# Kernel optimization log

Hardware: AMD Instinct MI355X
Metric: run time of the kernel (lower is better)

Reference implementation:

```python
import jax, jax.numpy as jnp
import numpy as np

HIDDEN = 1024
HEADS = 16
HEAD_DIM = HIDDEN // HEADS
FF = 4 * HIDDEN
B, S = 2, 2048


def _linear_params(key, out_dim, in_dim):
    kw, kb = jax.random.split(key)
    bound = 1.0 / np.sqrt(in_dim)
    W = jax.random.uniform(kw, (out_dim, in_dim), jnp.float32, -bound, bound)
    b = jax.random.uniform(kb, (out_dim,), jnp.float32, -bound, bound)
    return W, b


def setup_inputs() -> dict:
    key = jax.random.key(0)
    ks = jax.random.split(key, 8)
    x = jax.random.normal(ks[0], (B, S, HIDDEN), jnp.float32)
    attention_mask = jnp.ones((B, S), jnp.float32)
    Wq, bq = _linear_params(ks[1], HIDDEN, HIDDEN)
    Wk, bk = _linear_params(ks[2], HIDDEN, HIDDEN)
    Wv, bv = _linear_params(ks[3], HIDDEN, HIDDEN)
    Wo, bo = _linear_params(ks[4], HIDDEN, HIDDEN)
    W1, b1 = _linear_params(ks[5], FF, HIDDEN)
    W2, b2 = _linear_params(ks[6], HIDDEN, FF)
    g1 = jnp.ones((HIDDEN,), jnp.float32); be1 = jnp.zeros((HIDDEN,), jnp.float32)
    g2 = jnp.ones((HIDDEN,), jnp.float32); be2 = jnp.zeros((HIDDEN,), jnp.float32)
    return dict(x=x, attention_mask=attention_mask,
                Wq=Wq, bq=bq, Wk=Wk, bk=bk, Wv=Wv, bv=bv, Wo=Wo, bo=bo,
                W1=W1, b1=b1, W2=W2, b2=b2,
                g1=g1, be1=be1, g2=g2, be2=be2)


def _layer_norm(x, g, b, eps=1e-5):
    mu = jnp.mean(x, axis=-1, keepdims=True)
    var = jnp.mean(jnp.square(x - mu), axis=-1, keepdims=True)
    return (x - mu) * jax.lax.rsqrt(var + eps) * g + b


def reference(x, attention_mask, Wq, bq, Wk, bk, Wv, bv, Wo, bo,
              W1, b1, W2, b2, g1, be1, g2, be2):
    # Dropout is identity (eval mode / deterministic reference).
    residual = x
    h = _layer_norm(x, g1, be1)
    # [B,S,H] -> [B,nH,S,dh]
    def heads(t):
        return t.reshape(B, S, HEADS, HEAD_DIM).transpose(0, 2, 1, 3)
    q = heads(h @ Wq.T + bq)
    k = heads(h @ Wk.T + bk)
    v = heads(h @ Wv.T + bv)
    scores = jnp.einsum('bhqd,bhkd->bhqk', q, k) / np.sqrt(HEAD_DIM).astype(np.float32)
    scores = scores + (attention_mask[:, None, None, :] - 1.0) * 10000.0
    attn = jax.nn.softmax(scores, axis=-1)
    ctx = jnp.einsum('bhqk,bhkd->bhqd', attn, v)
    ctx = ctx.transpose(0, 2, 1, 3).reshape(B, S, HIDDEN)
    attn_out = ctx @ Wo.T + bo
    x = residual + attn_out
    residual = x
    h = _layer_norm(x, g2, be2)
    h = jax.nn.gelu(h @ W1.T + b1, approximate=False)
    h = h @ W2.T + b2
    return residual + h
```

## Files before the change

kernel.cpp:

```cpp
#include <hip/hip_runtime.h>
#include <hip/hip_bf16.h>
#include <math.h>

typedef __bf16 bf16;
typedef __bf16 bf16x4v __attribute__((ext_vector_type(4)));
typedef __bf16 bf16x8 __attribute__((ext_vector_type(8)));
typedef float  f32x4  __attribute__((ext_vector_type(4)));

#define HIDDEN 1024
#define TOKENS 4096
#define FFDIM  4096
#define SEQ    2048
#define NHEAD  16

#define LOG2E 1.44269504088896340736f

__device__ __forceinline__ void async_copy16(bf16* lds, const bf16* g)
{
    __builtin_amdgcn_global_load_lds(
        (__attribute__((address_space(1))) void*)g,
        (__attribute__((address_space(3))) void*)lds,
        16, 0, 0);
}

__global__ __launch_bounds__(256) void cvt_all_kernel(const float* __restrict__ wq,
    const float* __restrict__ wk, const float* __restrict__ wv, const float* __restrict__ wo,
    const float* __restrict__ w1, const float* __restrict__ w2, bf16* __restrict__ out)
{
    size_t i = ((size_t)blockIdx.x * 256 + threadIdx.x) * 4;
    int sel = (int)(i >> 20);
    const float* src;
    size_t off;
    if (sel < 4) { src = (sel == 0) ? wq : (sel == 1) ? wk : (sel == 2) ? wv : wo; off = i & ((1u << 20) - 1); }
    else if (sel < 8) { src = w1; off = i - ((size_t)4 << 20); }
    else              { src = w2; off = i - ((size_t)8 << 20); }
    float4 v = *(const float4*)&src[off];
    bf16x4v o = { (bf16)v.x, (bf16)v.y, (bf16)v.z, (bf16)v.w };
    *(bf16x4v*)&out[i] = o;
}

__global__ __launch_bounds__(256) void concat_bias_kernel(const float* __restrict__ bq,
    const float* __restrict__ bk, const float* __restrict__ bv, float* __restrict__ o)
{
    int i = blockIdx.x * 256 + threadIdx.x;
    float v = (i < 1024) ? bq[i] : (i < 2048 ? bk[i - 1024] : bv[i - 2048]);
    o[i] = v;
}

__global__ __launch_bounds__(256) void ln_kernel(const float* __restrict__ in,
    const float* __restrict__ g, const float* __restrict__ be, bf16* __restrict__ out)
{
    int row = blockIdx.x;
    int tid = threadIdx.x;
    const float* x = in + (size_t)row * HIDDEN;
    int i0 = tid * 4;
    float4 v = *(const float4*)&x[i0];
    float s  = v.x + v.y + v.z + v.w;
    float s2 = v.x*v.x + v.y*v.y + v.z*v.z + v.w*v.w;
    #pragma unroll
    for (int off = 32; off > 0; off >>= 1) { s += __shfl_xor(s, off); s2 += __shfl_xor(s2, off); }
    __shared__ float red[2][4];
    int wave = tid >> 6;
    if ((tid & 63) == 0) { red[0][wave] = s; red[1][wave] = s2; }
    __syncthreads();
    float ts  = red[0][0] + red[0][1] + red[0][2] + red[0][3];
    float ts2 = red[1][0] + red[1][1] + red[1][2] + red[1][3];
    float mu   = ts  * (1.0f / HIDDEN);
    float var  = ts2 * (1.0f / HIDDEN) - mu * mu;
    float rstd = rsqrtf(var + 1e-5f);
    float4 gg = *(const float4*)&g[i0];
    float4 bb = *(const float4*)&be[i0];
    bf16x4v o;
    o[0] = (bf16)((v.x - mu) * rstd * gg.x + bb.x);
    o[1] = (bf16)((v.y - mu) * rstd * gg.y + bb.y);
    o[2] = (bf16)((v.z - mu) * rstd * gg.z + bb.z);
    o[3] = (bf16)((v.w - mu) * rstd * gg.w + bb.w);
    *(bf16x4v*)&out[(size_t)row * HIDDEN + i0] = o;
}

template<int BM, int EPI, typename OT>
__global__ __launch_bounds__(256) void gemm_bt(const bf16* __restrict__ A, const bf16* __restrict__ Bt,
    const float* __restrict__ bias, const float* __restrict__ res, OT* __restrict__ C,
    int M, int N, int K)
{
    constexpr int MT = BM / 32;
    __shared__ bf16 As[BM * 64];
    __shared__ bf16 Bs[128 * 64];
    int tid  = threadIdx.x;
    int wave = tid >> 6, lane = tid & 63;
    int lm = lane & 15, quad = lane >> 4;
    int m0 = blockIdx.x * BM, n0 = blockIdx.y * 128;
    int wm = (wave >> 1) * (MT * 16), wn = (wave & 1) * 64;
    int r8 = lane >> 3, c8 = lane & 7;
    int gsw = (c8 ^ (r8 & 7)) * 8;
    f32x4 acc[MT][4] = {};
    for (int k0 = 0; k0 < K; k0 += 64) {
        #pragma unroll
        for (int ch = wave; ch < BM / 8; ch += 4)
            async_copy16(As + ch * 512, &A[(size_t)(m0 + ch * 8 + r8) * K + k0 + gsw]);
        #pragma unroll
        for (int ch = wave; ch < 16; ch += 4)
            async_copy16(Bs + ch * 512, &Bt[(size_t)(n0 + ch * 8 + r8) * K + k0 + gsw]);
        __syncthreads();
        bf16x8 af[MT][2], bfr[4][2];
        #pragma unroll
        for (int ks = 0; ks < 2; ks++) {
            int co = ((ks * 4 + quad) ^ (lm & 7)) * 8;
            #pragma unroll
            for (int t = 0; t < MT; t++) af[t][ks]  = *(const bf16x8*)&As[(wm + t * 16 + lm) * 64 + co];
            #pragma unroll
            for (int t = 0; t < 4; t++)  bfr[t][ks] = *(const bf16x8*)&Bs[(wn + t * 16 + lm) * 64 + co];
        }
        #pragma unroll
        for (int mt = 0; mt < MT; mt++)
            #pragma unroll
            for (int nt = 0; nt < 4; nt++)
                #pragma unroll
                for (int ks = 0; ks < 2; ks++)
                    acc[mt][nt] = __builtin_amdgcn_mfma_f32_16x16x32_bf16(af[mt][ks], bfr[nt][ks], acc[mt][nt], 0, 0, 0);
        __syncthreads();
    }
    #pragma unroll
    for (int mt = 0; mt < MT; mt++) {
        #pragma unroll
        for (int nt = 0; nt < 4; nt++) {
            int col = n0 + wn + nt * 16 + lm;
            float bv = bias[col];
            #pragma unroll
            for (int r = 0; r < 4; r++) {
                int row = m0 + wm + mt * 16 + quad * 4 + r;
                float vv = acc[mt][nt][r] + bv;
                if (EPI == 1) vv = 0.5f * vv * (1.0f + erff(vv * 0.70710678118654752f));
                if (EPI == 2) vv += res[(size_t)row * N + col];
                C[(size_t)row * N + col] = (OT)vv;
            }
        }
    }
}

__global__ __launch_bounds__(256) void gemm_qkv(const bf16* __restrict__ A, const bf16* __restrict__ W,
    const float* __restrict__ bias, bf16* __restrict__ qb, bf16* __restrict__ kb, bf16* __restrict__ vt)
{
    constexpr int K = HIDDEN;
    __shared__ bf16 As[128 * 64];
    __shared__ bf16 Bs[128 * 64];
    int tid  = threadIdx.x;
    int wave = tid >> 6, lane = tid & 63;
    int lm = lane & 15, quad = lane >> 4;
    int m0 = blockIdx.x * 128, n0 = blockIdx.y * 128;
    int wm = (wave >> 1) * 64, wn = (wave & 1) * 64;
    int r8 = lane >> 3, c8 = lane & 7;
    int gsw = (c8 ^ (r8 & 7)) * 8;
    f32x4 acc[4][4] = {};
    for (int k0 = 0; k0 < K; k0 += 64) {
        #pragma unroll
        for (int ch = wave; ch < 16; ch += 4) {
            async_copy16(As + ch * 512, &A[(size_t)(m0 + ch * 8 + r8) * K + k0 + gsw]);
            async_copy16(Bs + ch * 512, &W[(size_t)(n0 + ch * 8 + r8) * K + k0 + gsw]);
        }
        __syncthreads();
        bf16x8 af[4][2], bfr[4][2];
        #pragma unroll
        for (int ks = 0; ks < 2; ks++) {
            int co = ((ks * 4 + quad) ^ (lm & 7)) * 8;
            #pragma unroll
            for (int t = 0; t < 4; t++) {
                af[t][ks]  = *(const bf16x8*)&As[(wm + t * 16 + lm) * 64 + co];
                bfr[t][ks] = *(const bf16x8*)&Bs[(wn + t * 16 + lm) * 64 + co];
            }
        }
        #pragma unroll
        for (int mt = 0; mt < 4; mt++)
            #pragma unroll
            for (int nt = 0; nt < 4; nt++)
                #pragma unroll
                for (int ks = 0; ks < 2; ks++)
                    acc[mt][nt] = __builtin_amdgcn_mfma_f32_16x16x32_bf16(af[mt][ks], bfr[nt][ks], acc[mt][nt], 0, 0, 0);
        __syncthreads();
    }
    int region = n0 >> 10;
    #pragma unroll
    for (int mt = 0; mt < 4; mt++) {
        #pragma unroll
        for (int nt = 0; nt < 4; nt++) {
            int col = n0 + wn + nt * 16 + lm;
            float bv = bias[col];
            int cl = col & 1023;
            #pragma unroll
            for (int r = 0; r < 4; r++) {
                int row = m0 + wm + mt * 16 + quad * 4 + r;
                float vv = acc[mt][nt][r] + bv;
                if (region == 0)      qb[(size_t)row * HIDDEN + cl] = (bf16)vv;
                else if (region == 1) kb[(size_t)row * HIDDEN + cl] = (bf16)vv;
                else {
                    int h = cl >> 6, d = cl & 63;
                    int b = row >> 11, s = row & 2047;
                    vt[(((size_t)(b * NHEAD + h)) * 64 + d) * SEQ + s] = (bf16)vv;
                }
            }
        }
    }
}

__global__ __launch_bounds__(512) void attn_kernel(const bf16* __restrict__ Q, const bf16* __restrict__ K,
    const bf16* __restrict__ Vt, const float* __restrict__ mask, bf16* __restrict__ O)
{
    __shared__ bf16 Ks[2][64 * 64];
    __shared__ bf16 Vs[2][64 * 64];
    __shared__ bf16 Ps[8][16 * 72];
    int tid = threadIdx.x, wave = tid >> 6, lane = tid & 63;
    int lm = lane & 15, quad = lane >> 4;
    int bh = blockIdx.y, b = bh >> 4, h = bh & 15;
    int q0 = blockIdx.x * 128 + wave * 16;
    const size_t base  = ((size_t)b * SEQ) * HIDDEN + h * 64;
    const size_t vbase = (size_t)bh * 64 * SEQ;
    int srow8 = lane >> 3, spos = lane & 7;
    bf16x8 qf[2];
    #pragma unroll
    for (int ks = 0; ks < 2; ks++)
        qf[ks] = *(const bf16x8*)&Q[base + (size_t)(q0 + lm) * HIDDEN + ks * 32 + quad * 8];
    bf16x8 onesf;
    #pragma unroll
    for (int i = 0; i < 8; i++) onesf[i] = (bf16)1.0f;
    f32x4 o[4] = {};
    f32x4 lacc = {};
    const float c0 = 0.125f * LOG2E;
    const float cmk = 10000.0f * LOG2E;
    const float coff = -(cmk + 16.0f);
    bf16* pw = &Ps[wave][0];
    int r = wave * 8 + srow8;
    int gc = spos ^ (r & 7);
    auto stage = [&](int buf, int kt) {
        async_copy16(&Ks[buf][wave * 512], &K [base  + (size_t)(kt + r) * HIDDEN + gc * 8]);
        async_copy16(&Vs[buf][wave * 512], &Vt[vbase + (size_t)r * SEQ + kt + gc * 8]);
    };
    stage(0, 0);
    for (int ti = 0; ti < SEQ / 64; ti++) {
        __syncthreads();
        if (ti + 1 < SEQ / 64) stage((ti + 1) & 1, (ti + 1) * 64);
        const bf16* ksb = Ks[ti & 1];
        const bf16* vsb = Vs[ti & 1];
        int kt = ti * 64;
        f32x4 st[4] = {};
        #pragma unroll
        for (int nt = 0; nt < 4; nt++) {
            #pragma unroll
            for (int ks = 0; ks < 2; ks++) {
                bf16x8 kf = *(const bf16x8*)&ksb[(nt * 16 + lm) * 64 + (((ks * 4 + quad) ^ (lm & 7)) * 8)];
                st[nt] = __builtin_amdgcn_mfma_f32_16x16x32_bf16(kf, qf[ks], st[nt], 0, 0, 0);
            }
        }
        #pragma unroll
        for (int nt = 0; nt < 4; nt++) {
            float4 mv = *(const float4*)&mask[b * SEQ + kt + nt * 16 + quad * 4];
            float p0 = __builtin_amdgcn_exp2f(st[nt][0] * c0 + (mv.x * cmk + coff));
            float p1 = __builtin_amdgcn_exp2f(st[nt][1] * c0 + (mv.y * cmk + coff));
            float p2 = __builtin_amdgcn_exp2f(st[nt][2] * c0 + (mv.z * cmk + coff));
            float p3 = __builtin_amdgcn_exp2f(st[nt][3] * c0 + (mv.w * cmk + coff));
            bf16x4v pk = { (bf16)p0, (bf16)p1, (bf16)p2, (bf16)p3 };
            *(bf16x4v*)&pw[lm * 72 + nt * 16 + quad * 4] = pk;
        }
        bf16x8 pf[2];
        #pragma unroll
        for (int ks = 0; ks < 2; ks++)
            pf[ks] = *(const bf16x8*)&pw[lm * 72 + ks * 32 + quad * 8];
        lacc = __builtin_amdgcn_mfma_f32_16x16x32_bf16(pf[0], onesf, lacc, 0, 0, 0);
        lacc = __builtin_amdgcn_mfma_f32_16x16x32_bf16(pf[1], onesf, lacc, 0, 0, 0);
        #pragma unroll
        for (int dt = 0; dt < 4; dt++) {
            #pragma unroll
            for (int ks = 0; ks < 2; ks++) {
                bf16x8 vf = *(const bf16x8*)&vsb[(dt * 16 + lm) * 64 + (((ks * 4 + quad) ^ (lm & 7)) * 8)];
                o[dt] = __builtin_amdgcn_mfma_f32_16x16x32_bf16(pf[ks], vf, o[dt], 0, 0, 0);
            }
        }
    }
    #pragma unroll
    for (int rr = 0; rr < 4; rr++) {
        float inv = 1.0f / lacc[rr];
        #pragma unroll
        for (int dt = 0; dt < 4; dt++) {
            float val = o[dt][rr] * inv;
            O[base + (size_t)(q0 + quad * 4 + rr) * HIDDEN + dt * 16 + lm] = (bf16)val;
        }
    }
}

extern "C" void kernel_launch(void* const* d_in, const int* in_sizes, int n_in,
                              void* d_out, int out_size, void* d_ws, size_t ws_size,
                              hipStream_t stream)
{
    (void)in_sizes; (void)n_in; (void)out_size; (void)ws_size;
    const float* x    = (const float*)d_in[0];
    const float* mask = (const float*)d_in[1];
    const float* Wq   = (const float*)d_in[2];
    const float* bq   = (const float*)d_in[3];
    const float* Wk   = (const float*)d_in[4];
    const float* bk   = (const float*)d_in[5];
    const float* Wv   = (const float*)d_in[6];
    const float* bv   = (const float*)d_in[7];
    const float* Wo   = (const float*)d_in[8];
    const float* bo   = (const float*)d_in[9];
    const float* W1   = (const float*)d_in[10];
    const float* b1   = (const float*)d_in[11];
    const float* W2   = (const float*)d_in[12];
    const float* b2   = (const float*)d_in[13];
    const float* g1   = (const float*)d_in[14];
    const float* be1  = (const float*)d_in[15];
    const float* g2   = (const float*)d_in[16];
    const float* be2  = (const float*)d_in[17];
    float* out = (float*)d_out;

    const size_t M1 = 1024u * 1024u;
    bf16* ws    = (bf16*)d_ws;
    bf16* Wqkv_b = ws;
    bf16* Wo_b  = ws + 3 * M1;
    bf16* W1_b  = ws + 4 * M1;
    bf16* W2_b  = ws + 8 * M1;
    bf16* qb    = ws + 12 * M1;
    bf16* kb    = ws + 16 * M1;
    bf16* vt    = ws + 20 * M1;
    bf16* cx    = ws + 24 * M1;
    bf16* h     = ws + 28 * M1;
    bf16* ffb   = ws + 12 * M1;
    float* biasqkv = (float*)(ws + 24 * M1);

    cvt_all_kernel<<<dim3(12288), 256, 0, stream>>>(Wq, Wk, Wv, Wo, W1, W2, Wqkv_b);
    concat_bias_kernel<<<dim3(12), 256, 0, stream>>>(bq, bk, bv, biasqkv);

    ln_kernel<<<dim3(TOKENS), 256, 0, stream>>>(x, g1, be1, h);
    gemm_qkv<<<dim3(32, 24), 256, 0, stream>>>(h, Wqkv_b, biasqkv, qb, kb, vt);
    attn_kernel<<<dim3(SEQ / 128, 32), 512, 0, stream>>>(qb, kb, vt, mask, cx);
    gemm_bt<64, 2, float><<<dim3(64, 8), 256, 0, stream>>>(cx, Wo_b, bo, x, out, TOKENS, HIDDEN, HIDDEN);
    ln_kernel<<<dim3(TOKENS), 256, 0, stream>>>(out, g2, be2, h);
    gemm_bt<128, 1, bf16><<<dim3(32, 32), 256, 0, stream>>>(h, W1_b, b1, nullptr, ffb, TOKENS, FFDIM, HIDDEN);
    gemm_bt<64, 2, float><<<dim3(64, 8), 256, 0, stream>>>(ffb, W2_b, b2, out, out, TOKENS, HIDDEN, FFDIM);
}
```

Baseline: 384.5 us.

## Split attention over key halves with combine kernel; fold bias concat into convert

The attention kernel is templated on a key-split factor. With split 2 it launches twice as many blocks, each covering half the keys, and writes unnormalized fp32 partial outputs and row sums to workspace. A new combine kernel adds the two halves, normalizes them and writes bf16 context. This raises the block count from 512 to 1024 on a GPU with many CUs, at the cost of extra fp32 global traffic and one more launch. The bias concatenation also moves into extra blocks of the weight-convert kernel, removing one launch.

Result: slower. 402.7 us (+4.7%).

```diff
diff --git a/kernel.cpp b/kernel.cpp
--- a/kernel.cpp
+++ b/kernel.cpp
@@ -25,8 +25,16 @@
 
 __global__ __launch_bounds__(256) void cvt_all_kernel(const float* __restrict__ wq,
     const float* __restrict__ wk, const float* __restrict__ wv, const float* __restrict__ wo,
-    const float* __restrict__ w1, const float* __restrict__ w2, bf16* __restrict__ out)
-{
+    const float* __restrict__ w1, const float* __restrict__ w2, bf16* __restrict__ out,
+    const float* __restrict__ bq, const float* __restrict__ bk, const float* __restrict__ bv,
+    float* __restrict__ biasqkv)
+{
+    if (blockIdx.x >= 12288) {
+        int i = (blockIdx.x - 12288) * 256 + threadIdx.x;
+        float v = (i < 1024) ? bq[i] : (i < 2048 ? bk[i - 1024] : bv[i - 2048]);
+        biasqkv[i] = v;
+        return;
+    }
     size_t i = ((size_t)blockIdx.x * 256 + threadIdx.x) * 4;
     int sel = (int)(i >> 20);
     const float* src;
@@ -37,14 +45,6 @@
     float4 v = *(const float4*)&src[off];
     bf16x4v o = { (bf16)v.x, (bf16)v.y, (bf16)v.z, (bf16)v.w };
     *(bf16x4v*)&out[i] = o;
-}
-
-__global__ __launch_bounds__(256) void concat_bias_kernel(const float* __restrict__ bq,
-    const float* __restrict__ bk, const float* __restrict__ bv, float* __restrict__ o)
-{
-    int i = blockIdx.x * 256 + threadIdx.x;
-    float v = (i < 1024) ? bq[i] : (i < 2048 ? bk[i - 1024] : bv[i - 2048]);
-    o[i] = v;
 }
 
 __global__ __launch_bounds__(256) void ln_kernel(const float* __restrict__ in,
@@ -202,8 +202,10 @@
     }
 }
 
+template<int NSPLIT>
 __global__ __launch_bounds__(512) void attn_kernel(const bf16* __restrict__ Q, const bf16* __restrict__ K,
-    const bf16* __restrict__ Vt, const float* __restrict__ mask, bf16* __restrict__ O)
+    const bf16* __restrict__ Vt, const float* __restrict__ mask, bf16* __restrict__ O,
+    float* __restrict__ po, float* __restrict__ ls)
 {
     __shared__ bf16 Ks[2][64 * 64];
     __shared__ bf16 Vs[2][64 * 64];
@@ -211,6 +213,9 @@
     int tid = threadIdx.x, wave = tid >> 6, lane = tid & 63;
     int lm = lane & 15, quad = lane >> 4;
     int bh = blockIdx.y, b = bh >> 4, h = bh & 15;
+    int split = (NSPLIT == 2) ? blockIdx.z : 0;
+    int kbase = split * (SEQ / NSPLIT);
+    constexpr int NT = SEQ / 64 / NSPLIT;
     int q0 = blockIdx.x * 128 + wave * 16;
     const size_t base  = ((size_t)b * SEQ) * HIDDEN + h * 64;
     const size_t vbase = (size_t)bh * 64 * SEQ;
@@ -234,13 +239,13 @@
         async_copy16(&Ks[buf][wave * 512], &K [base  + (size_t)(kt + r) * HIDDEN + gc * 8]);
         async_copy16(&Vs[buf][wave * 512], &Vt[vbase + (size_t)r * SEQ + kt + gc * 8]);
     };
-    stage(0, 0);
-    for (int ti = 0; ti < SEQ / 64; ti++) {
-        __syncthreads();
-        if (ti + 1 < SEQ / 64) stage((ti + 1) & 1, (ti + 1) * 64);
+    stage(0, kbase);
+    for (int ti = 0; ti < NT; ti++) {
+        __syncthreads();
+        if (ti + 1 < NT) stage((ti + 1) & 1, kbase + (ti + 1) * 64);
         const bf16* ksb = Ks[ti & 1];
         const bf16* vsb = Vs[ti & 1];
-        int kt = ti * 64;
+        int kt = kbase + ti * 64;
         f32x4 st[4] = {};
         #pragma unroll
         for (int nt = 0; nt < 4; nt++) {
@@ -275,22 +280,54 @@
             }
         }
     }
-    #pragma unroll
-    for (int rr = 0; rr < 4; rr++) {
-        float inv = 1.0f / lacc[rr];
-        #pragma unroll
-        for (int dt = 0; dt < 4; dt++) {
-            float val = o[dt][rr] * inv;
-            O[base + (size_t)(q0 + quad * 4 + rr) * HIDDEN + dt * 16 + lm] = (bf16)val;
-        }
-    }
+    if (NSPLIT == 1) {
+        #pragma unroll
+        for (int rr = 0; rr < 4; rr++) {
+            float inv = 1.0f / lacc[rr];
+            #pragma unroll
+            for (int dt = 0; dt < 4; dt++) {
+                float val = o[dt][rr] * inv;
+                O[base + (size_t)(q0 + quad * 4 + rr) * HIDDEN + dt * 16 + lm] = (bf16)val;
+            }
+        }
+    } else {
+        float* pob = po + ((size_t)(split * 32 + bh) * SEQ) * 64;
+        float* lsb = ls + (size_t)(split * 32 + bh) * SEQ;
+        #pragma unroll
+        for (int rr = 0; rr < 4; rr++) {
+            int q = q0 + quad * 4 + rr;
+            if (lm == 0) lsb[q] = lacc[rr];
+            #pragma unroll
+            for (int dt = 0; dt < 4; dt++)
+                pob[(size_t)q * 64 + dt * 16 + lm] = o[dt][rr];
+        }
+    }
+}
+
+__global__ __launch_bounds__(256) void attn_combine(const float* __restrict__ po,
+    const float* __restrict__ ls, bf16* __restrict__ cx)
+{
+    const size_t HALF = (size_t)32 * SEQ * 64;
+    size_t e = ((size_t)blockIdx.x * 256 + threadIdx.x) * 4;
+    int d0 = (int)(e & 63);
+    size_t rem = e >> 6;
+    int s  = (int)(rem & (SEQ - 1));
+    int bh = (int)(rem >> 11);
+    float l = ls[(size_t)bh * SEQ + s] + ls[(size_t)(32 + bh) * SEQ + s];
+    float inv = 1.0f / l;
+    float4 a = *(const float4*)&po[e];
+    float4 c = *(const float4*)&po[HALF + e];
+    int b = bh >> 4, h = bh & 15;
+    bf16x4v o2 = { (bf16)((a.x + c.x) * inv), (bf16)((a.y + c.y) * inv),
+                   (bf16)((a.z + c.z) * inv), (bf16)((a.w + c.w) * inv) };
+    *(bf16x4v*)&cx[((size_t)(b * SEQ + s)) * HIDDEN + h * 64 + d0] = o2;
 }
 
 extern "C" void kernel_launch(void* const* d_in, const int* in_sizes, int n_in,
                               void* d_out, int out_size, void* d_ws, size_t ws_size,
                               hipStream_t stream)
 {
-    (void)in_sizes; (void)n_in; (void)out_size; (void)ws_size;
+    (void)in_sizes; (void)n_in; (void)out_size;
     const float* x    = (const float*)d_in[0];
     const float* mask = (const float*)d_in[1];
     const float* Wq   = (const float*)d_in[2];
@@ -324,13 +361,22 @@
     bf16* h     = ws + 28 * M1;
     bf16* ffb   = ws + 12 * M1;
     float* biasqkv = (float*)(ws + 24 * M1);
-
-    cvt_all_kernel<<<dim3(12288), 256, 0, stream>>>(Wq, Wk, Wv, Wo, W1, W2, Wqkv_b);
-    concat_bias_kernel<<<dim3(12), 256, 0, stream>>>(bq, bk, bv, biasqkv);
+    float* po = (float*)(ws + 32 * M1);
+    float* lsp = (float*)(ws + 50 * M1);
+    const size_t NEED = (size_t)106 * 1024 * 1024;
+    bool use_split = (ws_size >= NEED);
+
+    cvt_all_kernel<<<dim3(12300), 256, 0, stream>>>(Wq, Wk, Wv, Wo, W1, W2, Wqkv_b,
+                                                    bq, bk, bv, biasqkv);
 
     ln_kernel<<<dim3(TOKENS), 256, 0, stream>>>(x, g1, be1, h);
     gemm_qkv<<<dim3(32, 24), 256, 0, stream>>>(h, Wqkv_b, biasqkv, qb, kb, vt);
-    attn_kernel<<<dim3(SEQ / 128, 32), 512, 0, stream>>>(qb, kb, vt, mask, cx);
+    if (use_split) {
+        attn_kernel<2><<<dim3(SEQ / 128, 32, 2), 512, 0, stream>>>(qb, kb, vt, mask, cx, po, lsp);
+        attn_combine<<<dim3(4096), 256, 0, stream>>>(po, lsp, cx);
+    } else {
+        attn_kernel<1><<<dim3(SEQ / 128, 32, 1), 512, 0, stream>>>(qb, kb, vt, mask, cx, nullptr, nullptr);
+    }
     gemm_bt<64, 2, float><<<dim3(64, 8), 256, 0, stream>>>(cx, Wo_b, bo, x, out, TOKENS, HIDDEN, HIDDEN);
     ln_kernel<<<dim3(TOKENS), 256, 0, stream>>>(out, g2, be2, h);
     gemm_bt<128, 1, bf16><<<dim3(32, 32), 256, 0, stream>>>(h, W1_b, b1, nullptr, ffb, TOKENS, FFDIM, HIDDEN);
```
